# Performance work log

Measured on AMD Instinct MI355X. Metric: run time of the kernel, lower is better.

Reference implementation:

```python
import jax, jax.numpy as jnp
import numpy as np

EMBED_DIM = 1024
NUM_HEADS = 16
D_K = EMBED_DIM // NUM_HEADS
BATCH, SEQ = 4, 2048


def setup_inputs() -> dict:
    key = jax.random.key(0)
    ks = jax.random.split(key, 6)
    s = 1.0 / np.sqrt(EMBED_DIM)
    return {
        "x": jax.random.normal(ks[0], (BATCH, SEQ, EMBED_DIM), dtype=jnp.float32),
        "mask": jnp.ones((BATCH, SEQ), dtype=jnp.int32),
        "Wq": jax.random.uniform(ks[1], (EMBED_DIM, EMBED_DIM), jnp.float32, -s, s),
        "Wk": jax.random.uniform(ks[2], (EMBED_DIM, EMBED_DIM), jnp.float32, -s, s),
        "Wv": jax.random.uniform(ks[3], (EMBED_DIM, EMBED_DIM), jnp.float32, -s, s),
        "Wo": jax.random.uniform(ks[4], (EMBED_DIM, EMBED_DIM), jnp.float32, -s, s),
    }


def reference(x, mask, Wq, Wk, Wv, Wo):
    B, S, E = x.shape
    H, Dk = NUM_HEADS, D_K
    # nn.Linear: y = x @ W.T ; reshape to [B, H, S, Dk]
    def proj(W):
        return jnp.einsum('bse,fe->bsf', x, W).reshape(B, S, H, Dk).transpose(0, 2, 1, 3)
    q, k, v = proj(Wq), proj(Wk), proj(Wv)
    scores = jnp.einsum('bhqd,bhkd->bhqk', q, k) / jnp.sqrt(jnp.float32(Dk))
    # key-padding mask: [B, S] -> [B, 1, 1, S]; 0 means masked with -inf
    scores = jnp.where(mask[:, None, None, :] == 0, -jnp.inf, scores)
    attn = jax.nn.softmax(scores, axis=-1)  # dropout is identity (p=0 / eval)
    out = jnp.einsum('bhqk,bhkd->bhqd', attn, v)
    out = out.transpose(0, 2, 1, 3).reshape(B, S, E)
    return jnp.einsum('bse,fe->bsf', out, Wo)
```

## Files before the change

### kernel.cpp

```cpp
#include <hip/hip_runtime.h>

typedef __attribute__((ext_vector_type(8))) __bf16   bf16x8;
typedef __attribute__((ext_vector_type(8))) _Float16 f16x8;
typedef __attribute__((ext_vector_type(2))) __fp16   h16x2;
typedef __attribute__((ext_vector_type(8))) __fp16   h16x8;
typedef __attribute__((ext_vector_type(4))) float    f32x4;

#define MFMA_BF16 __builtin_amdgcn_mfma_f32_16x16x32_bf16
#define MFMA_F16  __builtin_amdgcn_mfma_f32_16x16x32_f16

__global__ __launch_bounds__(256)
void cast_bf16(const float* __restrict__ src, __bf16* __restrict__ dst, int n8)
{
    int i = blockIdx.x * 256 + threadIdx.x;
    if (i >= n8) return;
    float4 v0 = *(const float4*)(src + (size_t)i * 8);
    float4 v1 = *(const float4*)(src + (size_t)i * 8 + 4);
    float xs[8] = {v0.x, v0.y, v0.z, v0.w, v1.x, v1.y, v1.z, v1.w};
    bf16x8 h8;
    #pragma unroll
    for (int j = 0; j < 8; j++) h8[j] = (__bf16)xs[j];
    *(bf16x8*)(dst + (size_t)i * 8) = h8;
}

__global__ __launch_bounds__(256)
void mask_bias(const int* __restrict__ mask, float* __restrict__ bias, int n)
{
    int i = blockIdx.x * 256 + threadIdx.x;
    if (i < n) bias[i] = mask[i] ? 0.f : -30000.f;
}

#define GEMM_DECLS                                                          \
    __shared__ __bf16 Ah[128][40], Bh[128][40];                             \
    const int t    = threadIdx.x;                                           \
    const int lane = t & 63;                                                \
    const int wid  = t >> 6;                                                \
    const int l15  = lane & 15;                                             \
    const int lg   = lane >> 4;                                             \
    const int wr   = wid >> 1, wc = wid & 1;

#define GEMM_LOOP(Ag, Bg, m0, brow0, K)                                     \
    f32x4 acc[4][4];                                                        \
    _Pragma("unroll")                                                       \
    for (int i = 0; i < 4; i++)                                             \
        _Pragma("unroll")                                                   \
        for (int jj = 0; jj < 4; jj++)                                      \
            _Pragma("unroll")                                               \
            for (int r = 0; r < 4; r++) acc[i][jj][r] = 0.f;                \
    for (int k0 = 0; k0 < K; k0 += 32) {                                    \
        __syncthreads();                                                    \
        _Pragma("unroll")                                                   \
        for (int i = 0; i < 2; i++) {                                       \
            int id = t + 256 * i;                                           \
            int row = id >> 2, cc = id & 3;                                 \
            *(bf16x8*)&Ah[row][cc*8] =                                      \
                *(const bf16x8*)(Ag + (size_t)(m0 + row) * K + k0 + cc*8);  \
            *(bf16x8*)&Bh[row][cc*8] =                                      \
                *(const bf16x8*)(Bg + (size_t)(brow0 + row) * K + k0 + cc*8);\
        }                                                                   \
        __syncthreads();                                                    \
        bf16x8 ah[4];                                                       \
        _Pragma("unroll")                                                   \
        for (int mr = 0; mr < 4; mr++)                                      \
            ah[mr] = *(const bf16x8*)&Ah[wr*64 + mr*16 + l15][lg*8];        \
        _Pragma("unroll")                                                   \
        for (int nr = 0; nr < 4; nr++) {                                    \
            bf16x8 bh = *(const bf16x8*)&Bh[wc*64 + nr*16 + l15][lg*8];     \
            _Pragma("unroll")                                               \
            for (int mr = 0; mr < 4; mr++)                                  \
                acc[mr][nr] = MFMA_BF16(ah[mr], bh, acc[mr][nr], 0, 0, 0);  \
        }                                                                   \
    }

__global__ __launch_bounds__(256, 4)
void gemm_qkv(const __bf16* __restrict__ xh, const __bf16* __restrict__ w3,
              __bf16* __restrict__ qh, __bf16* __restrict__ kh,
              _Float16* __restrict__ vh)
{
    GEMM_DECLS
    const int K = 1024, N = 1024;
    const int m0     = blockIdx.x * 128;
    const int by     = blockIdx.y;
    const int region = by >> 3;
    const int n0     = (by & 7) * 128;
    const int brow0  = region * 1024 + n0;
    GEMM_LOOP(xh, w3, m0, brow0, K)

    constexpr float QSCALE = 0.18033688011112f;
    #pragma unroll
    for (int mr = 0; mr < 4; mr++)
    #pragma unroll
    for (int r = 0; r < 4; r++) {
        int row = m0 + wr*64 + mr*16 + lg*4 + r;
        #pragma unroll
        for (int nr = 0; nr < 4; nr++) {
            int col = n0 + wc*64 + nr*16 + l15;
            size_t off = (size_t)row * N + col;
            float v = acc[mr][nr][r];
            if (region == 0)      qh[off] = (__bf16)(v * QSCALE);
            else if (region == 1) kh[off] = (__bf16)v;
            else                  vh[off] = (_Float16)v;
        }
    }
}

__global__ __launch_bounds__(256, 4)
void gemm_out(const __bf16* __restrict__ aoh, const __bf16* __restrict__ woh,
              float* __restrict__ out, int M, int N, int K)
{
    GEMM_DECLS
    const int m0 = blockIdx.x * 128, n0 = blockIdx.y * 128;
    GEMM_LOOP(aoh, woh, m0, n0, K)

    #pragma unroll
    for (int mr = 0; mr < 4; mr++)
    #pragma unroll
    for (int r = 0; r < 4; r++) {
        int row = m0 + wr*64 + mr*16 + lg*4 + r;
        #pragma unroll
        for (int nr = 0; nr < 4; nr++) {
            int col = n0 + wc*64 + nr*16 + l15;
            out[(size_t)row * N + col] = acc[mr][nr][r];
        }
    }
}

__global__ __launch_bounds__(256, 2)
void attn_bf16(const __bf16* __restrict__ Qg, const __bf16* __restrict__ Kg,
               const _Float16* __restrict__ Vg, const float* __restrict__ biasg,
               __bf16* AO)
{
    const int S = 2048, E = 1024;
    __shared__ __align__(16) char smem[20736];
    __bf16   (*Kh)[72] = (__bf16 (*)[72])smem;
    _Float16 (*Vt)[72] = (_Float16 (*)[72])(smem + 9216);

    const int tid  = threadIdx.x;
    const int lane = tid & 63;
    const int wid  = tid >> 6;
    const int l15  = lane & 15;
    const int lg   = lane >> 4;

    const int fid = blockIdx.x;
    const int xcd = fid & 7;
    const int j   = fid >> 3;
    const int bh  = xcd * 8 + (j >> 4);
    const int qb  = j & 15;
    const int h   = bh & 15;
    const int b   = bh >> 4;
    const int q0  = qb * 128;
    const size_t base = (size_t)b * S * E + (size_t)h * 64;

    {
        _Float16* vones = &Vt[64][0];
        for (int i = tid; i < 16 * 72; i += 256) vones[i] = (_Float16)1.0f;
    }

    bf16x8 qf[2][2];
    #pragma unroll
    for (int mg = 0; mg < 2; mg++) {
        size_t qoff = base + (size_t)(q0 + wid*32 + mg*16 + l15) * E;
        #pragma unroll
        for (int kc = 0; kc < 2; kc++)
            qf[mg][kc] = *(const bf16x8*)(Qg + qoff + kc*32 + lg*8);
    }

    f32x4 o[2][4], osum[2];
    #pragma unroll
    for (int mg = 0; mg < 2; mg++) {
        #pragma unroll
        for (int nt = 0; nt < 4; nt++)
            #pragma unroll
            for (int r = 0; r < 4; r++) o[mg][nt][r] = 0.f;
        #pragma unroll
        for (int r = 0; r < 4; r++) osum[mg][r] = 0.f;
    }

    bf16x8 kpre[2]; f16x8 vpre[2];
    #pragma unroll
    for (int i = 0; i < 2; i++) {
        int id = tid + 256 * i, row = id >> 3, scc = id & 7;
        size_t g0 = base + (size_t)(row) * E + scc * 8;
        kpre[i] = *(const bf16x8*)(Kg + g0);
        vpre[i] = *(const f16x8*)(Vg + g0);
    }

    const int NT = S / 64;
    for (int t = 0; t < NT; t++) {
        const int k0 = t * 64;
        __syncthreads();

        #pragma unroll
        for (int i = 0; i < 2; i++) {
            int id = tid + 256 * i, row = id >> 3, scc = id & 7;
            *(bf16x8*)&Kh[row][scc*8] = kpre[i];
            int sg   = ((row & 12) >> 2) * 8 + ((row >> 4) & 1) * 4
                     + (row & 3) + (row & 32);
            int colw = (((sg >> 3) ^ scc) << 3) + (sg & 7);
            #pragma unroll
            for (int jj = 0; jj < 8; jj++)
                Vt[scc*8 + jj][colw] = vpre[i][jj];
        }

        if (t + 1 < NT) {
            #pragma unroll
            for (int i = 0; i < 2; i++) {
                int id = tid + 256 * i, row = id >> 3, scc = id & 7;
                size_t gn = base + (size_t)(k0 + 64 + row) * E + scc * 8;
                kpre[i] = *(const bf16x8*)(Kg + gn);
                vpre[i] = *(const f16x8*)(Vg + gn);
            }
        }
        __syncthreads();

        f32x4 sf[2][4];
        #pragma unroll
        for (int kvb = 0; kvb < 4; kvb++) {
            f32x4 bias4 = *(const f32x4*)(biasg + b * S + k0 + kvb*16 + lg*4);
            sf[0][kvb] = bias4;
            sf[1][kvb] = bias4;
        }
        #pragma unroll
        for (int kc = 0; kc < 2; kc++)
            #pragma unroll
            for (int kvb = 0; kvb < 4; kvb++) {
                bf16x8 kb = *(const bf16x8*)&Kh[kvb*16 + l15][kc*32 + lg*8];
                #pragma unroll
                for (int mg = 0; mg < 2; mg++)
                    sf[mg][kvb] = MFMA_BF16(kb, qf[mg][kc], sf[mg][kvb], 0, 0, 0);
            }

        f16x8 pa[2][2];
        #pragma unroll
        for (int mg = 0; mg < 2; mg++) {
            float p[4][4];
            #pragma unroll
            for (int kvb = 0; kvb < 4; kvb++)
                #pragma unroll
                for (int r = 0; r < 4; r++)
                    p[kvb][r] = __builtin_amdgcn_exp2f(sf[mg][kvb][r]);
            #pragma unroll
            for (int hh = 0; hh < 2; hh++) {
                h16x2 c0 = __builtin_amdgcn_cvt_pkrtz(p[2*hh][0],   p[2*hh][1]);
                h16x2 c1 = __builtin_amdgcn_cvt_pkrtz(p[2*hh][2],   p[2*hh][3]);
                h16x2 c2 = __builtin_amdgcn_cvt_pkrtz(p[2*hh+1][0], p[2*hh+1][1]);
                h16x2 c3 = __builtin_amdgcn_cvt_pkrtz(p[2*hh+1][2], p[2*hh+1][3]);
                h16x8 t8 = __builtin_shufflevector(
                    __builtin_shufflevector(c0, c1, 0, 1, 2, 3),
                    __builtin_shufflevector(c2, c3, 0, 1, 2, 3),
                    0, 1, 2, 3, 4, 5, 6, 7);
                pa[mg][hh] = __builtin_bit_cast(f16x8, t8);
            }
        }

        #pragma unroll
        for (int hh = 0; hh < 2; hh++) {
            #pragma unroll
            for (int nt = 0; nt < 4; nt++) {
                int c8p = (hh*4 + lg) ^ (nt*2 + (l15 >> 3));
                f16x8 vb = *(const f16x8*)&Vt[nt*16 + l15][c8p*8];
                o[0][nt] = MFMA_F16(pa[0][hh], vb, o[0][nt], 0, 0, 0);
                o[1][nt] = MFMA_F16(pa[1][hh], vb, o[1][nt], 0, 0, 0);
            }
            f16x8 vb1 = *(const f16x8*)&Vt[64 + l15][(hh*4 + lg)*8];
            osum[0] = MFMA_F16(pa[0][hh], vb1, osum[0], 0, 0, 0);
            osum[1] = MFMA_F16(pa[1][hh], vb1, osum[1], 0, 0, 0);
        }
    }

    float inv[2][4];
    #pragma unroll
    for (int mg = 0; mg < 2; mg++)
        #pragma unroll
        for (int r = 0; r < 4; r++) inv[mg][r] = 1.0f / osum[mg][r];

    unsigned short* Pu = (unsigned short*)smem;
    __syncthreads();
    #pragma unroll
    for (int mg = 0; mg < 2; mg++)
        #pragma unroll
        for (int r = 0; r < 4; r++)
            #pragma unroll
            for (int nt = 0; nt < 4; nt++) {
                __bf16 v = (__bf16)(o[mg][nt][r] * inv[mg][r]);
                Pu[(wid*32 + mg*16 + lg*4 + r) * 72 + nt*16 + l15] =
                    *(unsigned short*)&v;
            }
    __syncthreads();
    #pragma unroll
    for (int i = 0; i < 4; i++) {
        int u   = tid + 256 * i;
        int row = u >> 3, c8 = u & 7;
        bf16x8 v8;
        #pragma unroll
        for (int jj = 0; jj < 8; jj++) {
            unsigned short us = Pu[row * 72 + c8*8 + jj];
            v8[jj] = *(__bf16*)&us;
        }
        *(bf16x8*)(AO + base + (size_t)(q0 + row) * E + c8 * 8) = v8;
    }
}

extern "C" void kernel_launch(void* const* d_in, const int* in_sizes, int n_in,
                              void* d_out, int out_size, void* d_ws, size_t ws_size,
                              hipStream_t stream)
{
    const float* x    = (const float*)d_in[0];
    const int*   mask = (const int*)  d_in[1];
    const float* Wq   = (const float*)d_in[2];
    const float* Wk   = (const float*)d_in[3];
    const float* Wv   = (const float*)d_in[4];
    const float* Wo   = (const float*)d_in[5];
    float* out = (float*)d_out;

    const int B = 4, S = 2048, E = 1024;
    const int M = B * S;
    const size_t SZ  = (size_t)M * E;
    const size_t WSZ = (size_t)E * E;
    const size_t PB  = SZ * sizeof(__bf16);

    char* ws = (char*)d_ws;
    __bf16*   qh = (__bf16*)(ws);
    __bf16*   kh = (__bf16*)(ws + PB);
    _Float16* vh = (_Float16*)(ws + 2*PB);
    __bf16*   xh = (__bf16*)(ws + 3*PB);
    __bf16*   w3 = (__bf16*)(ws + 4*PB);
    __bf16*   wo = (__bf16*)(ws + 4*PB + 3*WSZ*sizeof(__bf16));
    float*    bs = (float*)(ws + 4*PB + 4*WSZ*sizeof(__bf16));

    const int n8x = (int)(SZ / 8);
    const int n8w = (int)(WSZ / 8);

    cast_bf16<<<n8x/256, 256, 0, stream>>>(x,  xh, n8x);
    cast_bf16<<<n8w/256, 256, 0, stream>>>(Wq, w3,           n8w);
    cast_bf16<<<n8w/256, 256, 0, stream>>>(Wk, w3 + WSZ,     n8w);
    cast_bf16<<<n8w/256, 256, 0, stream>>>(Wv, w3 + 2*WSZ,   n8w);
    cast_bf16<<<n8w/256, 256, 0, stream>>>(Wo, wo, n8w);
    mask_bias<<<(B*S)/256, 256, 0, stream>>>(mask, bs, B*S);

    gemm_qkv<<<dim3(M/128, 24), dim3(256), 0, stream>>>(xh, w3, qh, kh, vh);

    attn_bf16<<<dim3(1024), dim3(256), 0, stream>>>(qh, kh, vh, bs, qh);

    gemm_out<<<dim3(M/128, E/128), dim3(256), 0, stream>>>(qh, wo, out, M, E, E);
}
```

Measured before the change: 206.8 us.

## Fuse prep kernels, widen attention blocks, double-buffer K/V and drop ones row

Merges the five cast launches and the mask-bias launch into a single prep kernel. Attention blocks now use 512 threads covering 256 query rows each, so every K/V tile loaded into shared memory is reused by twice as many queries. K/V shared tiles are double-buffered, which removes one barrier per iteration. The row-sum MFMA now takes a register vector of ones instead of a ones row stored in shared memory. Shared memory per block grows, and fewer, larger blocks may reduce occupancy or latency hiding.

```diff
diff --git a/kernel.cpp b/kernel.cpp
--- a/kernel.cpp
+++ b/kernel.cpp
@@ -10,24 +10,41 @@
 #define MFMA_F16  __builtin_amdgcn_mfma_f32_16x16x32_f16
 
 __global__ __launch_bounds__(256)
-void cast_bf16(const float* __restrict__ src, __bf16* __restrict__ dst, int n8)
-{
-    int i = blockIdx.x * 256 + threadIdx.x;
-    if (i >= n8) return;
-    float4 v0 = *(const float4*)(src + (size_t)i * 8);
-    float4 v1 = *(const float4*)(src + (size_t)i * 8 + 4);
-    float xs[8] = {v0.x, v0.y, v0.z, v0.w, v1.x, v1.y, v1.z, v1.w};
-    bf16x8 h8;
-    #pragma unroll
-    for (int j = 0; j < 8; j++) h8[j] = (__bf16)xs[j];
-    *(bf16x8*)(dst + (size_t)i * 8) = h8;
-}
-
-__global__ __launch_bounds__(256)
-void mask_bias(const int* __restrict__ mask, float* __restrict__ bias, int n)
-{
-    int i = blockIdx.x * 256 + threadIdx.x;
-    if (i < n) bias[i] = mask[i] ? 0.f : -30000.f;
+void prep_all(const float* __restrict__ x,  const float* __restrict__ Wq,
+              const float* __restrict__ Wk, const float* __restrict__ Wv,
+              const float* __restrict__ Wo, const int* __restrict__ mask,
+              __bf16* __restrict__ xh, __bf16* __restrict__ w3,
+              __bf16* __restrict__ wo, float* __restrict__ bias)
+{
+    const int i = blockIdx.x * 256 + threadIdx.x;
+    const int WSZ8 = 131072;
+
+    if (i < 1572864) {
+        const float* src; __bf16* dst; int o8;
+        if (i < 1048576)      { src = x;  dst = xh;            o8 = i; }
+        else if (i < 1179648) { src = Wq; dst = w3;            o8 = i - 1048576; }
+        else if (i < 1310720) { src = Wk; dst = w3 + 1048576;  o8 = i - 1179648; }
+        else if (i < 1441792) { src = Wv; dst = w3 + 2097152;  o8 = i - 1310720; }
+        else                  { src = Wo; dst = wo;            o8 = i - 1441792; }
+        float4 v0 = *(const float4*)(src + (size_t)o8 * 8);
+        float4 v1 = *(const float4*)(src + (size_t)o8 * 8 + 4);
+        float xs[8] = {v0.x, v0.y, v0.z, v0.w, v1.x, v1.y, v1.z, v1.w};
+        bf16x8 h8;
+        #pragma unroll
+        for (int jj = 0; jj < 8; jj++) h8[jj] = (__bf16)xs[jj];
+        *(bf16x8*)(dst + (size_t)o8 * 8) = h8;
+    } else {
+        int c = i - 1572864;
+        int4 m0 = *(const int4*)(mask + c * 8);
+        int4 m1 = *(const int4*)(mask + c * 8 + 4);
+        float4 b0, b1;
+        b0.x = m0.x ? 0.f : -30000.f;  b0.y = m0.y ? 0.f : -30000.f;
+        b0.z = m0.z ? 0.f : -30000.f;  b0.w = m0.w ? 0.f : -30000.f;
+        b1.x = m1.x ? 0.f : -30000.f;  b1.y = m1.y ? 0.f : -30000.f;
+        b1.z = m1.z ? 0.f : -30000.f;  b1.w = m1.w ? 0.f : -30000.f;
+        *(float4*)(bias + c * 8)     = b0;
+        *(float4*)(bias + c * 8 + 4) = b1;
+    }
 }
 
 #define GEMM_DECLS                                                          \
@@ -125,15 +142,13 @@
     }
 }
 
-__global__ __launch_bounds__(256, 2)
+__global__ __launch_bounds__(512, 2)
 void attn_bf16(const __bf16* __restrict__ Qg, const __bf16* __restrict__ Kg,
                const _Float16* __restrict__ Vg, const float* __restrict__ biasg,
                __bf16* AO)
 {
     const int S = 2048, E = 1024;
-    __shared__ __align__(16) char smem[20736];
-    __bf16   (*Kh)[72] = (__bf16 (*)[72])smem;
-    _Float16 (*Vt)[72] = (_Float16 (*)[72])(smem + 9216);
+    __shared__ __align__(16) char smem[36864];
 
     const int tid  = threadIdx.x;
     const int lane = tid & 63;
@@ -144,17 +159,12 @@
     const int fid = blockIdx.x;
     const int xcd = fid & 7;
     const int j   = fid >> 3;
-    const int bh  = xcd * 8 + (j >> 4);
-    const int qb  = j & 15;
+    const int bh  = xcd * 8 + (j >> 3);
+    const int qb  = j & 7;
     const int h   = bh & 15;
     const int b   = bh >> 4;
-    const int q0  = qb * 128;
+    const int q0  = qb * 256;
     const size_t base = (size_t)b * S * E + (size_t)h * 64;
-
-    {
-        _Float16* vones = &Vt[64][0];
-        for (int i = tid; i < 16 * 72; i += 256) vones[i] = (_Float16)1.0f;
-    }
 
     bf16x8 qf[2][2];
     #pragma unroll
@@ -176,40 +186,41 @@
         for (int r = 0; r < 4; r++) osum[mg][r] = 0.f;
     }
 
-    bf16x8 kpre[2]; f16x8 vpre[2];
-    #pragma unroll
-    for (int i = 0; i < 2; i++) {
-        int id = tid + 256 * i, row = id >> 3, scc = id & 7;
-        size_t g0 = base + (size_t)(row) * E + scc * 8;
-        kpre[i] = *(const bf16x8*)(Kg + g0);
-        vpre[i] = *(const f16x8*)(Vg + g0);
+    f16x8 ones8;
+    #pragma unroll
+    for (int jj = 0; jj < 8; jj++) ones8[jj] = (_Float16)1.0f;
+
+    const int srow = tid >> 3;
+    const int scc  = tid & 7;
+    const int sg   = ((srow & 12) >> 2) * 8 + ((srow >> 4) & 1) * 4
+                   + (srow & 3) + (srow & 32);
+
+    bf16x8 kpre; f16x8 vpre;
+    {
+        size_t g0 = base + (size_t)srow * E + scc * 8;
+        kpre = *(const bf16x8*)(Kg + g0);
+        vpre = *(const f16x8*)(Vg + g0);
     }
 
     const int NT = S / 64;
     for (int t = 0; t < NT; t++) {
         const int k0 = t * 64;
-        __syncthreads();
-
-        #pragma unroll
-        for (int i = 0; i < 2; i++) {
-            int id = tid + 256 * i, row = id >> 3, scc = id & 7;
-            *(bf16x8*)&Kh[row][scc*8] = kpre[i];
-            int sg   = ((row & 12) >> 2) * 8 + ((row >> 4) & 1) * 4
-                     + (row & 3) + (row & 32);
+        char* buf = smem + (t & 1) * 18432;
+        __bf16   (*Kh)[72] = (__bf16 (*)[72])buf;
+        _Float16 (*Vt)[72] = (_Float16 (*)[72])(buf + 9216);
+
+        *(bf16x8*)&Kh[srow][scc*8] = kpre;
+        {
             int colw = (((sg >> 3) ^ scc) << 3) + (sg & 7);
             #pragma unroll
             for (int jj = 0; jj < 8; jj++)
-                Vt[scc*8 + jj][colw] = vpre[i][jj];
+                Vt[scc*8 + jj][colw] = vpre[jj];
         }
 
         if (t + 1 < NT) {
-            #pragma unroll
-            for (int i = 0; i < 2; i++) {
-                int id = tid + 256 * i, row = id >> 3, scc = id & 7;
-                size_t gn = base + (size_t)(k0 + 64 + row) * E + scc * 8;
-                kpre[i] = *(const bf16x8*)(Kg + gn);
-                vpre[i] = *(const f16x8*)(Vg + gn);
-            }
+            size_t gn = base + (size_t)(k0 + 64 + srow) * E + scc * 8;
+            kpre = *(const bf16x8*)(Kg + gn);
+            vpre = *(const f16x8*)(Vg + gn);
         }
         __syncthreads();
 
@@ -262,9 +273,8 @@
                 o[0][nt] = MFMA_F16(pa[0][hh], vb, o[0][nt], 0, 0, 0);
                 o[1][nt] = MFMA_F16(pa[1][hh], vb, o[1][nt], 0, 0, 0);
             }
-            f16x8 vb1 = *(const f16x8*)&Vt[64 + l15][(hh*4 + lg)*8];
-            osum[0] = MFMA_F16(pa[0][hh], vb1, osum[0], 0, 0, 0);
-            osum[1] = MFMA_F16(pa[1][hh], vb1, osum[1], 0, 0, 0);
+            osum[0] = MFMA_F16(pa[0][hh], ones8, osum[0], 0, 0, 0);
+            osum[1] = MFMA_F16(pa[1][hh], ones8, osum[1], 0, 0, 0);
         }
     }
 
@@ -289,7 +299,7 @@
     __syncthreads();
     #pragma unroll
     for (int i = 0; i < 4; i++) {
-        int u   = tid + 256 * i;
+        int u   = tid + 512 * i;
         int row = u >> 3, c8 = u & 7;
         bf16x8 v8;
         #pragma unroll
@@ -328,19 +338,12 @@
     __bf16*   wo = (__bf16*)(ws + 4*PB + 3*WSZ*sizeof(__bf16));
     float*    bs = (float*)(ws + 4*PB + 4*WSZ*sizeof(__bf16));
 
-    const int n8x = (int)(SZ / 8);
-    const int n8w = (int)(WSZ / 8);
-
-    cast_bf16<<<n8x/256, 256, 0, stream>>>(x,  xh, n8x);
-    cast_bf16<<<n8w/256, 256, 0, stream>>>(Wq, w3,           n8w);
-    cast_bf16<<<n8w/256, 256, 0, stream>>>(Wk, w3 + WSZ,     n8w);
-    cast_bf16<<<n8w/256, 256, 0, stream>>>(Wv, w3 + 2*WSZ,   n8w);
-    cast_bf16<<<n8w/256, 256, 0, stream>>>(Wo, wo, n8w);
-    mask_bias<<<(B*S)/256, 256, 0, stream>>>(mask, bs, B*S);
+    prep_all<<<dim3(6148), dim3(256), 0, stream>>>(
+        x, Wq, Wk, Wv, Wo, mask, xh, w3, wo, bs);
 
     gemm_qkv<<<dim3(M/128, 24), dim3(256), 0, stream>>>(xh, w3, qh, kh, vh);
 
-    attn_bf16<<<dim3(1024), dim3(256), 0, stream>>>(qh, kh, vh, bs, qh);
+    attn_bf16<<<dim3(512), dim3(512), 0, stream>>>(qh, kh, vh, bs, qh);
 
     gemm_out<<<dim3(M/128, E/128), dim3(256), 0, stream>>>(qh, wo, out, M, E, E);
 }
```

Result: faster. 196.6 us (-4.9%).
